# Optimization experiments

Hardware: AMD Instinct MI355X
Metric: run time of the kernel (lower is better)

## Reference

```python
import jax, jax.numpy as jnp
import numpy as np

N, H, E, T = 100000, 128, 500000, 6  # nodes, hidden, max edges, edge types


def setup_inputs() -> dict:
    key = jax.random.key(0)
    ks = jax.random.split(key, 16)
    xav_e = float(np.sqrt(6.0 / (H + T * H)))  # xavier_uniform for edge_dense
    xav_h = float(np.sqrt(6.0 / (H + H)))
    u = lambda k, s, a: jax.random.uniform(k, s, jnp.float32, -a, a)
    return {
        "node_embeddings": jax.random.normal(ks[0], (N, H), jnp.float32),
        "W_edge": u(ks[1], (H, T * H), xav_e),
        "b_edge": 1e-6 * jax.random.normal(ks[2], (T * H,), jnp.float32),
        "W_ir": u(ks[3], (H, H), xav_h), "b_ir": jnp.zeros((H,), jnp.float32),
        "W_iz": u(ks[4], (H, H), xav_h), "b_iz": jnp.zeros((H,), jnp.float32),
        "W_in": u(ks[5], (H, H), xav_h), "b_in": jnp.zeros((H,), jnp.float32),
        "W_hr": u(ks[6], (H, H), xav_h),
        "W_hz": u(ks[7], (H, H), xav_h),
        "W_hn": u(ks[8], (H, H), xav_h), "b_hn": jnp.zeros((H,), jnp.float32),
        "source_indices": jax.random.randint(ks[9], (E,), 0, N, jnp.int32),
        "dest_indices": jax.random.randint(ks[10], (E,), 0, N, jnp.int32),
        "edge_types": jax.random.randint(ks[11], (E,), 0, T, jnp.int32),
        "num_edges": 450000,
    }


def reference(node_embeddings, W_edge, b_edge, W_ir, b_ir, W_iz, b_iz,
              W_in, b_in, W_hr, W_hz, W_hn, b_hn,
              source_indices, dest_indices, edge_types, num_edges):
    num_nodes, hidden = node_embeddings.shape
    max_edges = edge_types.shape[0]
    # gather source nodes, project to all edge types at once: [E, T*H]
    src = node_embeddings[source_indices]
    all_types = (src @ W_edge + b_edge).reshape(max_edges, -1, hidden)  # [E,T,H]
    # select per-edge type
    msg = jnp.take_along_axis(all_types, edge_types[:, None, None], axis=1)[:, 0, :]
    # mask padding edges, scatter-add into destination nodes
    msg = jnp.where((jnp.arange(max_edges) < num_edges)[:, None], msg, 0)
    agg = jax.ops.segment_sum(msg, dest_indices, num_segments=num_nodes)
    # GRU update: carry h = aggregated messages, inputs x = node_embeddings
    h, x = agg, node_embeddings
    r = jax.nn.sigmoid(x @ W_ir + b_ir + h @ W_hr)
    z = jax.nn.sigmoid(x @ W_iz + b_iz + h @ W_hz)
    n = jnp.tanh(x @ W_in + b_in + r * (h @ W_hn + b_hn))
    return (1.0 - z) * n + z * h
```

## Files before the change

kernel.cpp:

```cpp
#include <hip/hip_runtime.h>
#include <hip/hip_bf16.h>

#define HD 128
#define NT 6

typedef unsigned short u16;
typedef unsigned int u32;
typedef __attribute__((ext_vector_type(8))) short bf16x8;
typedef __attribute__((ext_vector_type(4))) float f32x4;

__device__ __forceinline__ float sigmoidf_(float x) {
  return 1.0f / (1.0f + __expf(-x));
}

__device__ __forceinline__ u16 f2bf(float x) {
  u32 u = __float_as_uint(x);
  return (u16)((u + 0x7FFFu + ((u >> 16) & 1u)) >> 16);
}
__device__ __forceinline__ float bflo(u32 v) { return __uint_as_float(v << 16); }
__device__ __forceinline__ float bfhi(u32 v) { return __uint_as_float(v & 0xffff0000u); }

__device__ __forceinline__ int swz(int p) { return p ^ (((p >> 8) & 7) << 4); }

__global__ void k_cvt_w(const float* __restrict__ We,
                        const float* __restrict__ Wir, const float* __restrict__ Wiz,
                        const float* __restrict__ Win, const float* __restrict__ Whr,
                        const float* __restrict__ Whz, const float* __restrict__ Whn,
                        u16* __restrict__ WeT, u16* __restrict__ WgT) {
  int i = blockIdx.x * blockDim.x + threadIdx.x;
  if (i < NT * HD * HD) {
    int c = i >> 7, k = i & 127;
    WeT[i] = f2bf(We[(size_t)k * (NT * HD) + c]);
  } else {
    int j = i - NT * HD * HD;
    if (j < 6 * HD * HD) {
      int m = j >> 14, jj = j & 16383;
      int c = jj >> 7, k = jj & 127;
      const float* W = (m == 0) ? Wir : (m == 1) ? Wiz : (m == 2) ? Win
                     : (m == 3) ? Whr : (m == 4) ? Whz : Whn;
      WgT[j] = f2bf(W[(size_t)k * HD + c]);
    }
  }
}

__global__ __launch_bounds__(256) void k_gemm_edge6(
    const float* __restrict__ X, const u16* __restrict__ WeT,
    const float* __restrict__ Be, u16* __restrict__ P, int N)
{
  __shared__ char As[32768];
  __shared__ char Bs[32768];
  const int tid = threadIdx.x;
  const int row0 = blockIdx.x * 128;

  #pragma unroll
  for (int i = 0; i < 8; ++i) {
    int p = i * 4096 + tid * 16;
    int row = row0 + (p >> 8);
    union { u16 u[8]; bf16x8 v; } ra;
    if (row < N) {
      const float4* s = (const float4*)(X + (size_t)row0 * HD + (p >> 1));
      float4 f0 = s[0], f1 = s[1];
      ra.u[0] = f2bf(f0.x); ra.u[1] = f2bf(f0.y); ra.u[2] = f2bf(f0.z); ra.u[3] = f2bf(f0.w);
      ra.u[4] = f2bf(f1.x); ra.u[5] = f2bf(f1.y); ra.u[6] = f2bf(f1.z); ra.u[7] = f2bf(f1.w);
    } else {
      #pragma unroll
      for (int j = 0; j < 8; ++j) ra.u[j] = 0;
    }
    *(bf16x8*)(As + swz(p)) = ra.v;
  }

  const int l = tid & 63, w = tid >> 6;
  const int m0 = (w >> 1) * 64, n0 = (w & 1) * 64;
  const int lr = l & 15, lg = l >> 4;
  f32x4 zero = {0.f, 0.f, 0.f, 0.f};

  for (int t = 0; t < NT; ++t) {
    __syncthreads();
    const char* gB = (const char*)(WeT + (size_t)t * HD * HD);
    #pragma unroll
    for (int i = 0; i < 8; ++i) {
      int p = i * 4096 + tid * 16;
      *(bf16x8*)(Bs + swz(p)) = *(const bf16x8*)(gB + p);
    }
    __syncthreads();

    f32x4 acc[4][4];
    #pragma unroll
    for (int m = 0; m < 4; ++m)
      #pragma unroll
      for (int n = 0; n < 4; ++n) acc[m][n] = zero;

    #pragma unroll
    for (int k = 0; k < 4; ++k) {
      bf16x8 a[4], b[4];
      #pragma unroll
      for (int m = 0; m < 4; ++m)
        a[m] = *(const bf16x8*)(As + swz((m0 + m * 16 + lr) * 256 + k * 64 + lg * 16));
      #pragma unroll
      for (int n = 0; n < 4; ++n)
        b[n] = *(const bf16x8*)(Bs + swz((n0 + n * 16 + lr) * 256 + k * 64 + lg * 16));
      #pragma unroll
      for (int m = 0; m < 4; ++m)
        #pragma unroll
        for (int n = 0; n < 4; ++n)
          acc[m][n] = __builtin_amdgcn_mfma_f32_16x16x32_bf16(a[m], b[n], acc[m][n], 0, 0, 0);
    }

    float bias[4];
    #pragma unroll
    for (int n = 0; n < 4; ++n) bias[n] = Be[t * HD + n0 + n * 16 + lr];
    #pragma unroll
    for (int m = 0; m < 4; ++m) {
      int rbase = row0 + m0 + m * 16 + lg * 4;
      #pragma unroll
      for (int j = 0; j < 4; ++j) {
        int row = rbase + j;
        if (row < N) {
          #pragma unroll
          for (int n = 0; n < 4; ++n)
            P[(size_t)row * (NT * HD) + t * HD + n0 + n * 16 + lr] =
                f2bf(acc[m][n][j] + bias[n]);
        }
      }
    }
  }
}

__global__ __launch_bounds__(256) void k_count(const int* __restrict__ dst,
                                               const int* __restrict__ nePtr,
                                               int* __restrict__ deg) {
  const int ne = nePtr[0];
  for (int e = blockIdx.x * blockDim.x + threadIdx.x; e < ne;
       e += gridDim.x * blockDim.x)
    atomicAdd(&deg[dst[e]], 1);
}

__global__ __launch_bounds__(256) void k_scan_a(const int* __restrict__ deg,
                                                int* __restrict__ off,
                                                int* __restrict__ bsum, int N) {
  __shared__ int s[256];
  const int b = blockIdx.x, tid = threadIdx.x;
  const int base = b * 1024 + tid * 4;
  int v0 = 0, v1 = 0, v2 = 0, v3 = 0;
  if (base < N) v0 = deg[base];
  if (base + 1 < N) v1 = deg[base + 1];
  if (base + 2 < N) v2 = deg[base + 2];
  if (base + 3 < N) v3 = deg[base + 3];
  const int sum = v0 + v1 + v2 + v3;
  s[tid] = sum;
  __syncthreads();
  for (int d = 1; d < 256; d <<= 1) {
    int t = (tid >= d) ? s[tid - d] : 0;
    __syncthreads();
    s[tid] += t;
    __syncthreads();
  }
  const int excl = s[tid] - sum;
  if (base < N) off[base] = excl;
  if (base + 1 < N) off[base + 1] = excl + v0;
  if (base + 2 < N) off[base + 2] = excl + v0 + v1;
  if (base + 3 < N) off[base + 3] = excl + v0 + v1 + v2;
  if (tid == 255) bsum[b] = s[255];
}

__global__ void k_scan_b(int* __restrict__ bsum, int nb) {
  __shared__ int s[1024];
  const int tid = threadIdx.x;
  const int v = (tid < nb) ? bsum[tid] : 0;
  s[tid] = v;
  __syncthreads();
  for (int d = 1; d < 1024; d <<= 1) {
    int t = (tid >= d) ? s[tid - d] : 0;
    __syncthreads();
    s[tid] += t;
    __syncthreads();
  }
  if (tid < nb) bsum[tid] = s[tid] - v;
}

__global__ __launch_bounds__(256) void k_scan_c(int* __restrict__ off,
                                                const int* __restrict__ bsum, int N) {
  const int b = blockIdx.x, tid = threadIdx.x;
  const int add = bsum[b];
  const int base = b * 1024 + tid * 4;
  #pragma unroll
  for (int i = 0; i < 4; ++i)
    if (base + i < N) off[base + i] += add;
}

__global__ __launch_bounds__(256) void k_fill(const int* __restrict__ src,
                                              const int* __restrict__ dst,
                                              const int* __restrict__ typ,
                                              const int* __restrict__ nePtr,
                                              int* __restrict__ off,
                                              u32* __restrict__ elist) {
  const int ne = nePtr[0];
  for (int e = blockIdx.x * blockDim.x + threadIdx.x; e < ne;
       e += gridDim.x * blockDim.x) {
    int pos = atomicAdd(&off[dst[e]], 1);
    elist[pos] = (u32)(src[e] * NT + typ[e]);
  }
}

__global__ __launch_bounds__(256) void k_gather(
    const u16* __restrict__ P, const int* __restrict__ deg,
    const int* __restrict__ off, const u32* __restrict__ elist,
    u16* __restrict__ Hb, int N)
{
  const int l = threadIdx.x & 63;
  int wid = (int)((blockIdx.x * blockDim.x + threadIdx.x) >> 6);
  int nw = (int)((gridDim.x * blockDim.x) >> 6);
  for (int n = wid; n < N; n += nw) {
    const int e1 = off[n];
    const int e0 = e1 - deg[n];
    float a0 = 0.f, a1 = 0.f, b0 = 0.f, b1 = 0.f;
    for (int e = e0; e < e1; e += 4) {
      u32 p0 = elist[e];
      u32 p1 = (e + 1 < e1) ? elist[e + 1] : p0;
      u32 p2 = (e + 2 < e1) ? elist[e + 2] : p0;
      u32 p3 = (e + 3 < e1) ? elist[e + 3] : p0;
      u32 v0 = *((const u32*)(P + (size_t)p0 * HD) + l);
      u32 v1 = *((const u32*)(P + (size_t)p1 * HD) + l);
      u32 v2 = *((const u32*)(P + (size_t)p2 * HD) + l);
      u32 v3 = *((const u32*)(P + (size_t)p3 * HD) + l);
      if (e + 1 >= e1) v1 = 0;
      if (e + 2 >= e1) v2 = 0;
      if (e + 3 >= e1) v3 = 0;
      a0 += bflo(v0); a1 += bfhi(v0);
      b0 += bflo(v1); b1 += bfhi(v1);
      a0 += bflo(v2); a1 += bfhi(v2);
      b0 += bflo(v3); b1 += bfhi(v3);
    }
    a0 += b0; a1 += b1;
    u32 hp = ((u32)f2bf(a1) << 16) | (u32)f2bf(a0);
    *((u32*)(Hb + (size_t)n * HD) + l) = hp;
  }
}

__global__ __launch_bounds__(512, 2) void k_gru3(
    const float* __restrict__ X, const u16* __restrict__ Hb,
    const u16* __restrict__ WgT,
    const float* __restrict__ bir, const float* __restrict__ biz,
    const float* __restrict__ bin_, const float* __restrict__ bhn,
    float* __restrict__ out, int N)
{
  __shared__ char Xs[32768];
  __shared__ char Hs[32768];
  __shared__ char Wb[2][32768];
  const int tid = threadIdx.x;
  const int row0 = blockIdx.x * 128;
  const int l = tid & 63, w = tid >> 6;
  const int lr = l & 15, lg = l >> 4;
  const int rloc = w * 16;

  #pragma unroll
  for (int i = 0; i < 4; ++i) {
    int p = i * 8192 + tid * 16;
    int row = row0 + (p >> 8);
    union { u16 u[8]; bf16x8 v; } rx, rh;
    if (row < N) {
      const float4* sx = (const float4*)(X + (size_t)row0 * HD + (p >> 1));
      float4 x0 = sx[0], x1 = sx[1];
      rx.u[0] = f2bf(x0.x); rx.u[1] = f2bf(x0.y); rx.u[2] = f2bf(x0.z); rx.u[3] = f2bf(x0.w);
      rx.u[4] = f2bf(x1.x); rx.u[5] = f2bf(x1.y); rx.u[6] = f2bf(x1.z); rx.u[7] = f2bf(x1.w);
      rh.v = *(const bf16x8*)((const char*)Hb + (size_t)row0 * 256 + p);
    } else {
      #pragma unroll
      for (int j = 0; j < 8; ++j) { rx.u[j] = 0; rh.u[j] = 0; }
    }
    *(bf16x8*)(Xs + swz(p)) = rx.v;
    *(bf16x8*)(Hs + swz(p)) = rh.v;
  }

  bf16x8 wreg[4];
  auto loadW = [&](int g) {
    const char* gp = (const char*)(WgT + (size_t)g * HD * HD);
    #pragma unroll
    for (int i = 0; i < 4; ++i)
      wreg[i] = *(const bf16x8*)(gp + i * 8192 + tid * 16);
  };
  auto writeW = [&](int buf) {
    #pragma unroll
    for (int i = 0; i < 4; ++i) {
      int p = i * 8192 + tid * 16;
      *(bf16x8*)(Wb[buf] + swz(p)) = wreg[i];
    }
  };

  f32x4 zero = {0.f, 0.f, 0.f, 0.f};
  auto sweepL = [&](const char* Ab, const char* Wp, f32x4* acc) {
    #pragma unroll
    for (int n = 0; n < 8; ++n) acc[n] = zero;
    #pragma unroll
    for (int k = 0; k < 4; ++k) {
      bf16x8 a = *(const bf16x8*)(Ab + swz((rloc + lr) * 256 + k * 64 + lg * 16));
      #pragma unroll
      for (int n = 0; n < 8; ++n) {
        bf16x8 b = *(const bf16x8*)(Wp + swz((n * 16 + lr) * 256 + k * 64 + lg * 16));
        acc[n] = __builtin_amdgcn_mfma_f32_16x16x32_bf16(a, b, acc[n], 0, 0, 0);
      }
    }
  };

  f32x4 t1[8], t2[8], rg[8], nn[8];
  float bv[8];

  loadW(0); writeW(0);
  __syncthreads();

  loadW(3);
  sweepL(Xs, Wb[0], t1);
  writeW(1);
  __syncthreads();

  loadW(5);
  sweepL(Hs, Wb[1], t2);
  writeW(0);
  #pragma unroll
  for (int n = 0; n < 8; ++n) bv[n] = bir[n * 16 + lr];
  #pragma unroll
  for (int n = 0; n < 8; ++n)
    #pragma unroll
    for (int j = 0; j < 4; ++j) rg[n][j] = sigmoidf_(t1[n][j] + bv[n] + t2[n][j]);
  __syncthreads();

  loadW(2);
  sweepL(Hs, Wb[0], t2);
  writeW(1);
  #pragma unroll
  for (int n = 0; n < 8; ++n) bv[n] = bhn[n * 16 + lr];
  #pragma unroll
  for (int n = 0; n < 8; ++n)
    #pragma unroll
    for (int j = 0; j < 4; ++j) rg[n][j] *= (t2[n][j] + bv[n]);
  __syncthreads();

  loadW(1);
  sweepL(Xs, Wb[1], t1);
  writeW(0);
  #pragma unroll
  for (int n = 0; n < 8; ++n) bv[n] = bin_[n * 16 + lr];
  #pragma unroll
  for (int n = 0; n < 8; ++n)
    #pragma unroll
    for (int j = 0; j < 4; ++j) nn[n][j] = tanhf(t1[n][j] + bv[n] + rg[n][j]);
  __syncthreads();

  loadW(4);
  sweepL(Xs, Wb[0], t1);
  writeW(1);
  __syncthreads();

  sweepL(Hs, Wb[1], t2);
  #pragma unroll
  for (int n = 0; n < 8; ++n) bv[n] = biz[n * 16 + lr];
  #pragma unroll
  for (int n = 0; n < 8; ++n) {
    #pragma unroll
    for (int j = 0; j < 4; ++j) {
      int row = row0 + rloc + lg * 4 + j;
      if (row < N) {
        int col = n * 16 + lr;
        float z = sigmoidf_(t1[n][j] + bv[n] + t2[n][j]);
        u16 hu = Hb[(size_t)row * HD + col];
        float h = __uint_as_float((u32)hu << 16);
        out[(size_t)row * HD + col] = (1.0f - z) * nn[n][j] + z * h;
      }
    }
  }
}

__global__ __launch_bounds__(256) void k_gather_gru(
    const float* __restrict__ X, const u16* __restrict__ P,
    const int* __restrict__ deg, const int* __restrict__ off,
    const u32* __restrict__ elist, const u16* __restrict__ WgT,
    const float* __restrict__ bir, const float* __restrict__ biz,
    const float* __restrict__ bin_, const float* __restrict__ bhn,
    float* __restrict__ out, int N)
{
  __shared__ char Xs[16384];
  __shared__ char Hs[16384];
  const int tid = threadIdx.x;
  const int l = tid & 63, w = tid >> 6;
  const int row0 = blockIdx.x * 64;
  const int wr0 = w * 16;

  #pragma unroll
  for (int it = 0; it < 4; ++it) {
    int chunk = it * 64 + l;
    int r = chunk >> 4, seg = chunk & 15;
    int grow = row0 + wr0 + r;
    union { u16 u[8]; bf16x8 v; } rx;
    if (grow < N) {
      const float4* sx = (const float4*)(X + (size_t)grow * HD + seg * 8);
      float4 x0 = sx[0], x1 = sx[1];
      rx.u[0] = f2bf(x0.x); rx.u[1] = f2bf(x0.y); rx.u[2] = f2bf(x0.z); rx.u[3] = f2bf(x0.w);
      rx.u[4] = f2bf(x1.x); rx.u[5] = f2bf(x1.y); rx.u[6] = f2bf(x1.z); rx.u[7] = f2bf(x1.w);
    } else {
      #pragma unroll
      for (int j = 0; j < 8; ++j) rx.u[j] = 0;
    }
    *(bf16x8*)(Xs + swz((wr0 + r) * 256 + seg * 16)) = rx.v;
  }

  for (int i = 0; i < 16; ++i) {
    int n = row0 + wr0 + i;
    float a0 = 0.f, a1 = 0.f;
    if (n < N) {
      int e1 = off[n];
      for (int e = e1 - deg[n]; e < e1; e += 4) {
        u32 p0 = elist[e];
        u32 p1 = (e + 1 < e1) ? elist[e + 1] : p0;
        u32 p2 = (e + 2 < e1) ? elist[e + 2] : p0;
        u32 p3 = (e + 3 < e1) ? elist[e + 3] : p0;
        u32 v0 = *((const u32*)(P + (size_t)p0 * HD) + l);
        u32 v1 = *((const u32*)(P + (size_t)p1 * HD) + l);
        u32 v2 = *((const u32*)(P + (size_t)p2 * HD) + l);
        u32 v3 = *((const u32*)(P + (size_t)p3 * HD) + l);
        if (e + 1 >= e1) v1 = 0;
        if (e + 2 >= e1) v2 = 0;
        if (e + 3 >= e1) v3 = 0;
        a0 += bflo(v0) + bflo(v1) + bflo(v2) + bflo(v3);
        a1 += bfhi(v0) + bfhi(v1) + bfhi(v2) + bfhi(v3);
      }
    }
    u32 hp = ((u32)f2bf(a1) << 16) | (u32)f2bf(a0);
    *(u32*)(Hs + swz((wr0 + i) * 256 + l * 4)) = hp;
  }

  const int lr = l & 15, lg = l >> 4;
  const int rloc = wr0;

  f32x4 zero = {0.f, 0.f, 0.f, 0.f};
  auto sweep = [&](const char* Ab, const u16* WT, f32x4* acc) {
    #pragma unroll
    for (int n = 0; n < 8; ++n) acc[n] = zero;
    #pragma unroll
    for (int k = 0; k < 4; ++k) {
      bf16x8 a = *(const bf16x8*)(Ab + swz((rloc + lr) * 256 + k * 64 + lg * 16));
      #pragma unroll
      for (int n = 0; n < 8; ++n) {
        bf16x8 b = *(const bf16x8*)(WT + (size_t)(n * 16 + lr) * HD + k * 32 + lg * 8);
        acc[n] = __builtin_amdgcn_mfma_f32_16x16x32_bf16(a, b, acc[n], 0, 0, 0);
      }
    }
  };

  f32x4 t1[8], t2[8], rg[8], nn[8];
  float bv[8];

  sweep(Xs, WgT + 0 * HD * HD, t1);
  sweep(Hs, WgT + 3 * HD * HD, t2);
  #pragma unroll
  for (int n = 0; n < 8; ++n) bv[n] = bir[n * 16 + lr];
  #pragma unroll
  for (int n = 0; n < 8; ++n)
    #pragma unroll
    for (int j = 0; j < 4; ++j) rg[n][j] = sigmoidf_(t1[n][j] + bv[n] + t2[n][j]);

  sweep(Hs, WgT + 5 * HD * HD, t2);
  #pragma unroll
  for (int n = 0; n < 8; ++n) bv[n] = bhn[n * 16 + lr];
  #pragma unroll
  for (int n = 0; n < 8; ++n)
    #pragma unroll
    for (int j = 0; j < 4; ++j) rg[n][j] *= (t2[n][j] + bv[n]);

  sweep(Xs, WgT + 2 * HD * HD, t1);
  #pragma unroll
  for (int n = 0; n < 8; ++n) bv[n] = bin_[n * 16 + lr];
  #pragma unroll
  for (int n = 0; n < 8; ++n)
    #pragma unroll
    for (int j = 0; j < 4; ++j) nn[n][j] = tanhf(t1[n][j] + bv[n] + rg[n][j]);

  sweep(Xs, WgT + 1 * HD * HD, t1);
  sweep(Hs, WgT + 4 * HD * HD, t2);
  #pragma unroll
  for (int n = 0; n < 8; ++n) bv[n] = biz[n * 16 + lr];
  #pragma unroll
  for (int n = 0; n < 8; ++n) {
    #pragma unroll
    for (int j = 0; j < 4; ++j) {
      int row = row0 + rloc + lg * 4 + j;
      if (row < N) {
        float z = sigmoidf_(t1[n][j] + bv[n] + t2[n][j]);
        u16 hu = *(const u16*)(Hs + swz((rloc + lg * 4 + j) * 256 + (n * 16 + lr) * 2));
        float h = __uint_as_float((u32)hu << 16);
        out[(size_t)row * HD + n * 16 + lr] = (1.0f - z) * nn[n][j] + z * h;
      }
    }
  }
}

__global__ __launch_bounds__(256) void k_scatter(
    const u16* __restrict__ P, const int* __restrict__ src,
    const int* __restrict__ dst, const int* __restrict__ typ,
    const int* __restrict__ nePtr, float* __restrict__ agg,
    int ldP, int fixedType)
{
  const int ne = nePtr[0];
  const int lane = threadIdx.x & 63;
  const int wid = (int)((blockIdx.x * blockDim.x + threadIdx.x) >> 6);
  const int nw = (int)((gridDim.x * blockDim.x) >> 6);
  for (int e = wid; e < ne; e += nw) {
    const int t = typ[e];
    if (fixedType >= 0 && t != fixedType) continue;
    const size_t po = (ldP == HD) ? (size_t)src[e] * HD
                                  : (size_t)src[e] * (NT * HD) + (size_t)t * HD;
    u32 v = *(const u32*)(P + po + lane * 2);
    float* o = agg + (size_t)dst[e] * HD + lane * 2;
    unsafeAtomicAdd(o, bflo(v));
    unsafeAtomicAdd(o + 1, bfhi(v));
  }
}

__global__ __launch_bounds__(256) void k_gru(
    const float* __restrict__ X, const float* __restrict__ agg,
    const u16* __restrict__ WgT,
    const float* __restrict__ bir, const float* __restrict__ biz,
    const float* __restrict__ bin_, const float* __restrict__ bhn,
    float* __restrict__ out, int N)
{
  __shared__ char Xs[16384];
  __shared__ char Hs[16384];
  const int tid = threadIdx.x;
  const int row0 = blockIdx.x * 64;

  #pragma unroll
  for (int i = 0; i < 4; ++i) {
    int p = i * 4096 + tid * 16;
    int row = row0 + (p >> 8);
    union { u16 u[8]; bf16x8 v; } rx, rh;
    if (row < N) {
      const float4* sx = (const float4*)(X + (size_t)row0 * HD + (p >> 1));
      const float4* sh = (const float4*)(agg + (size_t)row0 * HD + (p >> 1));
      float4 x0 = sx[0], x1 = sx[1], h0 = sh[0], h1 = sh[1];
      rx.u[0] = f2bf(x0.x); rx.u[1] = f2bf(x0.y); rx.u[2] = f2bf(x0.z); rx.u[3] = f2bf(x0.w);
      rx.u[4] = f2bf(x1.x); rx.u[5] = f2bf(x1.y); rx.u[6] = f2bf(x1.z); rx.u[7] = f2bf(x1.w);
      rh.u[0] = f2bf(h0.x); rh.u[1] = f2bf(h0.y); rh.u[2] = f2bf(h0.z); rh.u[3] = f2bf(h0.w);
      rh.u[4] = f2bf(h1.x); rh.u[5] = f2bf(h1.y); rh.u[6] = f2bf(h1.z); rh.u[7] = f2bf(h1.w);
    } else {
      #pragma unroll
      for (int j = 0; j < 8; ++j) { rx.u[j] = 0; rh.u[j] = 0; }
    }
    *(bf16x8*)(Xs + swz(p)) = rx.v;
    *(bf16x8*)(Hs + swz(p)) = rh.v;
  }
  __syncthreads();

  const int l = tid & 63, w = tid >> 6;
  const int lr = l & 15, lg = l >> 4;
  const int rloc = w * 16;

  f32x4 zero = {0.f, 0.f, 0.f, 0.f};
  auto sweep = [&](const char* Ab, const u16* WT, f32x4* acc) {
    #pragma unroll
    for (int n = 0; n < 8; ++n) acc[n] = zero;
    #pragma unroll
    for (int k = 0; k < 4; ++k) {
      bf16x8 a = *(const bf16x8*)(Ab + swz((rloc + lr) * 256 + k * 64 + lg * 16));
      #pragma unroll
      for (int n = 0; n < 8; ++n) {
        bf16x8 b = *(const bf16x8*)(WT + (size_t)(n * 16 + lr) * HD + k * 32 + lg * 8);
        acc[n] = __builtin_amdgcn_mfma_f32_16x16x32_bf16(a, b, acc[n], 0, 0, 0);
      }
    }
  };

  f32x4 t1[8], t2[8], rg[8], nn[8];
  float bv[8];

  sweep(Xs, WgT + 0 * HD * HD, t1);
  sweep(Hs, WgT + 3 * HD * HD, t2);
  #pragma unroll
  for (int n = 0; n < 8; ++n) bv[n] = bir[n * 16 + lr];
  #pragma unroll
  for (int n = 0; n < 8; ++n)
    #pragma unroll
    for (int j = 0; j < 4; ++j) rg[n][j] = sigmoidf_(t1[n][j] + bv[n] + t2[n][j]);

  sweep(Hs, WgT + 5 * HD * HD, t2);
  #pragma unroll
  for (int n = 0; n < 8; ++n) bv[n] = bhn[n * 16 + lr];
  #pragma unroll
  for (int n = 0; n < 8; ++n)
    #pragma unroll
    for (int j = 0; j < 4; ++j) rg[n][j] *= (t2[n][j] + bv[n]);

  sweep(Xs, WgT + 2 * HD * HD, t1);
  #pragma unroll
  for (int n = 0; n < 8; ++n) bv[n] = bin_[n * 16 + lr];
  #pragma unroll
  for (int n = 0; n < 8; ++n)
    #pragma unroll
    for (int j = 0; j < 4; ++j) nn[n][j] = tanhf(t1[n][j] + bv[n] + rg[n][j]);

  sweep(Xs, WgT + 1 * HD * HD, t1);
  sweep(Hs, WgT + 4 * HD * HD, t2);
  #pragma unroll
  for (int n = 0; n < 8; ++n) bv[n] = biz[n * 16 + lr];
  #pragma unroll
  for (int n = 0; n < 8; ++n) {
    #pragma unroll
    for (int j = 0; j < 4; ++j) {
      int row = row0 + rloc + lg * 4 + j;
      if (row < N) {
        float z = sigmoidf_(t1[n][j] + bv[n] + t2[n][j]);
        float h = agg[(size_t)row * HD + n * 16 + lr];
        out[(size_t)row * HD + n * 16 + lr] = (1.0f - z) * nn[n][j] + z * h;
      }
    }
  }
}

extern "C" void kernel_launch(void* const* d_in, const int* in_sizes, int n_in,
                              void* d_out, int out_size, void* d_ws, size_t ws_size,
                              hipStream_t stream) {
  const float* X      = (const float*)d_in[0];
  const float* W_edge = (const float*)d_in[1];
  const float* b_edge = (const float*)d_in[2];
  const float* b_ir   = (const float*)d_in[4];
  const float* b_iz   = (const float*)d_in[6];
  const float* b_in   = (const float*)d_in[8];
  const float* b_hn   = (const float*)d_in[12];
  const int* src      = (const int*)d_in[13];
  const int* dst      = (const int*)d_in[14];
  const int* typ      = (const int*)d_in[15];
  const int* nePtr    = (const int*)d_in[16];

  const int N = in_sizes[0] / HD;
  const int E = in_sizes[13];
  char* ws = (char*)d_ws;

  size_t cur = 0;
  auto alloc = [&](size_t bytes) {
    size_t p = cur;
    cur = (cur + bytes + 255) & ~(size_t)255;
    return p;
  };
  u16* WeT   = (u16*)(ws + alloc((size_t)NT * HD * HD * 2));
  u16* WgT   = (u16*)(ws + alloc((size_t)6 * HD * HD * 2));
  int* deg   = (int*)(ws + alloc((size_t)N * 4));
  int* offA  = (int*)(ws + alloc((size_t)N * 4));
  int* bsum  = (int*)(ws + alloc(1024 * 4));
  u32* elist = (u32*)(ws + alloc((size_t)E * 4));
  size_t base_need = cur;
  u16* P     = (u16*)(ws + alloc((size_t)N * NT * HD * 2));
  const size_t csr_need = cur;
  u16* Hb    = (u16*)(ws + alloc((size_t)N * HD * 2));
  const size_t split_need = cur;

  const int gb = (N + 127) / 128;
  const int NB = (N + 1023) / 1024;

  k_cvt_w<<<(NT * HD * HD + 6 * HD * HD + 255) / 256, 256, 0, stream>>>(
      W_edge, (const float*)d_in[3], (const float*)d_in[5], (const float*)d_in[7],
      (const float*)d_in[9], (const float*)d_in[10], (const float*)d_in[11], WeT, WgT);

  if (ws_size >= csr_need) {
    hipMemsetAsync(deg, 0, (size_t)N * 4, stream);
    k_gemm_edge6<<<gb, 256, 0, stream>>>(X, WeT, b_edge, P, N);
    k_count<<<1024, 256, 0, stream>>>(dst, nePtr, deg);
    k_scan_a<<<NB, 256, 0, stream>>>(deg, offA, bsum, N);
    k_scan_b<<<1, 1024, 0, stream>>>(bsum, NB);
    k_scan_c<<<NB, 256, 0, stream>>>(offA, bsum, N);
    k_fill<<<1024, 256, 0, stream>>>(src, dst, typ, nePtr, offA, elist);
    if (ws_size >= split_need) {
      k_gather<<<(N + 3) / 4, 256, 0, stream>>>(P, deg, offA, elist, Hb, N);
      k_gru3<<<gb, 512, 0, stream>>>(
          X, Hb, WgT, b_ir, b_iz, b_in, b_hn, (float*)d_out, N);
    } else {
      k_gather_gru<<<(N + 63) / 64, 256, 0, stream>>>(
          X, P, deg, offA, elist, WgT, b_ir, b_iz, b_in, b_hn, (float*)d_out, N);
    }
  } else {
    float* agg = (float*)d_out;
    hipMemsetAsync(d_out, 0, (size_t)out_size * sizeof(float), stream);
    size_t pneed = base_need + (size_t)N * NT * HD * 2;
    if (ws_size >= pneed) {
      u16* Pf = (u16*)(ws + base_need);
      k_gemm_edge6<<<gb, 256, 0, stream>>>(X, WeT, b_edge, Pf, N);
      k_scatter<<<2048, 256, 0, stream>>>(Pf, src, dst, typ, nePtr, agg, NT * HD, -1);
      k_gru<<<(N + 63) / 64, 256, 0, stream>>>(X, agg, WgT, b_ir, b_iz, b_in, b_hn, agg, N);
    }
  }
}
```

Measured before the change: 253.6 us.

## Emit bf16 copy of node embeddings in edge GEMM and use LDS-free GRU kernel

The edge-projection GEMM now also writes a bf16 copy of the node embeddings into workspace while it converts them. A new GRU kernel, k_gru4, reads that bf16 copy and the aggregated bf16 H directly from global memory into MFMA operands, with no shared-memory staging, in 32x64 wave tiles. The goal is to halve the X read traffic in the GRU stage and drop the LDS staging and barriers of k_gru3. In exchange it adds an extra write of X in bf16 and relies on cache hits for the repeated weight and activation loads across gate passes.

```diff
diff --git a/kernel.cpp b/kernel.cpp
--- a/kernel.cpp
+++ b/kernel.cpp
@@ -45,7 +45,8 @@
 
 __global__ __launch_bounds__(256) void k_gemm_edge6(
     const float* __restrict__ X, const u16* __restrict__ WeT,
-    const float* __restrict__ Be, u16* __restrict__ P, int N)
+    const float* __restrict__ Be, u16* __restrict__ P,
+    u16* __restrict__ Xb, int N)
 {
   __shared__ char As[32768];
   __shared__ char Bs[32768];
@@ -62,6 +63,7 @@
       float4 f0 = s[0], f1 = s[1];
       ra.u[0] = f2bf(f0.x); ra.u[1] = f2bf(f0.y); ra.u[2] = f2bf(f0.z); ra.u[3] = f2bf(f0.w);
       ra.u[4] = f2bf(f1.x); ra.u[5] = f2bf(f1.y); ra.u[6] = f2bf(f1.z); ra.u[7] = f2bf(f1.w);
+      if (Xb) *(bf16x8*)((char*)Xb + (size_t)row * 256 + (p & 255)) = ra.v;
     } else {
       #pragma unroll
       for (int j = 0; j < 8; ++j) ra.u[j] = 0;
@@ -237,6 +239,118 @@
   }
 }
 
+__global__ __launch_bounds__(256) void k_gru4(
+    const u16* __restrict__ Xb, const u16* __restrict__ Hb,
+    const u16* __restrict__ WgT,
+    const float* __restrict__ bir, const float* __restrict__ biz,
+    const float* __restrict__ bin_, const float* __restrict__ bhn,
+    float* __restrict__ out, int N)
+{
+  const int tid = threadIdx.x;
+  const int l = tid & 63;
+  const int lr = l & 15, lg = l >> 4;
+  const int gw = (int)(blockIdx.x * 4 + (tid >> 6));
+  const int R0 = (gw >> 1) * 32;
+  const int C0 = (gw & 1) * 64;
+  if (R0 >= N) return;
+
+  const bf16x8 zf = {0, 0, 0, 0, 0, 0, 0, 0};
+  f32x4 zero = {0.f, 0.f, 0.f, 0.f};
+
+  auto ldA = [&](const u16* Mb, int m, int kc) -> bf16x8 {
+    int row = R0 + m * 16 + lr;
+    if (row >= N) return zf;
+    return *(const bf16x8*)(Mb + (size_t)row * HD + kc * 32 + lg * 8);
+  };
+  auto ldB = [&](const u16* Wt, int n, int kc) -> bf16x8 {
+    return *(const bf16x8*)(Wt + (size_t)(C0 + n * 16 + lr) * HD + kc * 32 + lg * 8);
+  };
+
+  f32x4 t[2][4];
+  auto zeroT = [&]() {
+    #pragma unroll
+    for (int m = 0; m < 2; ++m)
+      #pragma unroll
+      for (int n = 0; n < 4; ++n) t[m][n] = zero;
+  };
+  auto pass = [&](const u16* Mb, const u16* Wt) {
+    #pragma unroll
+    for (int kc = 0; kc < 4; ++kc) {
+      bf16x8 a0 = ldA(Mb, 0, kc);
+      bf16x8 a1 = ldA(Mb, 1, kc);
+      #pragma unroll
+      for (int n = 0; n < 4; ++n) {
+        bf16x8 b = ldB(Wt, n, kc);
+        t[0][n] = __builtin_amdgcn_mfma_f32_16x16x32_bf16(a0, b, t[0][n], 0, 0, 0);
+        t[1][n] = __builtin_amdgcn_mfma_f32_16x16x32_bf16(a1, b, t[1][n], 0, 0, 0);
+      }
+    }
+  };
+
+  float bv[4];
+  auto ldBias = [&](const float* bp) {
+    #pragma unroll
+    for (int n = 0; n < 4; ++n) bv[n] = bp[C0 + n * 16 + lr];
+  };
+
+  float rg[2][4][4], nn[2][4][4];
+
+  zeroT();
+  pass(Xb, WgT + 0 * HD * HD);
+  pass(Hb, WgT + 3 * HD * HD);
+  ldBias(bir);
+  #pragma unroll
+  for (int m = 0; m < 2; ++m)
+    #pragma unroll
+    for (int n = 0; n < 4; ++n)
+      #pragma unroll
+      for (int j = 0; j < 4; ++j)
+        rg[m][n][j] = sigmoidf_(t[m][n][j] + bv[n]);
+
+  zeroT();
+  pass(Hb, WgT + 5 * HD * HD);
+  ldBias(bhn);
+  #pragma unroll
+  for (int m = 0; m < 2; ++m)
+    #pragma unroll
+    for (int n = 0; n < 4; ++n)
+      #pragma unroll
+      for (int j = 0; j < 4; ++j)
+        rg[m][n][j] *= (t[m][n][j] + bv[n]);
+
+  zeroT();
+  pass(Xb, WgT + 2 * HD * HD);
+  ldBias(bin_);
+  #pragma unroll
+  for (int m = 0; m < 2; ++m)
+    #pragma unroll
+    for (int n = 0; n < 4; ++n)
+      #pragma unroll
+      for (int j = 0; j < 4; ++j)
+        nn[m][n][j] = tanhf(t[m][n][j] + bv[n] + rg[m][n][j]);
+
+  zeroT();
+  pass(Xb, WgT + 1 * HD * HD);
+  pass(Hb, WgT + 4 * HD * HD);
+  ldBias(biz);
+  #pragma unroll
+  for (int m = 0; m < 2; ++m) {
+    #pragma unroll
+    for (int j = 0; j < 4; ++j) {
+      int row = R0 + m * 16 + lg * 4 + j;
+      if (row < N) {
+        #pragma unroll
+        for (int n = 0; n < 4; ++n) {
+          int col = C0 + n * 16 + lr;
+          float z = sigmoidf_(t[m][n][j] + bv[n]);
+          float h = __uint_as_float((u32)Hb[(size_t)row * HD + col] << 16);
+          out[(size_t)row * HD + col] = (1.0f - z) * nn[m][n][j] + z * h;
+        }
+      }
+    }
+  }
+}
+
 __global__ __launch_bounds__(512, 2) void k_gru3(
     const float* __restrict__ X, const u16* __restrict__ Hb,
     const u16* __restrict__ WgT,
@@ -650,6 +764,8 @@
   const size_t csr_need = cur;
   u16* Hb    = (u16*)(ws + alloc((size_t)N * HD * 2));
   const size_t split_need = cur;
+  u16* Xb    = (u16*)(ws + alloc((size_t)N * HD * 2));
+  const size_t xb_need = cur;
 
   const int gb = (N + 127) / 128;
   const int NB = (N + 1023) / 1024;
@@ -659,14 +775,20 @@
       (const float*)d_in[9], (const float*)d_in[10], (const float*)d_in[11], WeT, WgT);
 
   if (ws_size >= csr_need) {
+    const bool haveXb = (ws_size >= xb_need);
     hipMemsetAsync(deg, 0, (size_t)N * 4, stream);
-    k_gemm_edge6<<<gb, 256, 0, stream>>>(X, WeT, b_edge, P, N);
+    k_gemm_edge6<<<gb, 256, 0, stream>>>(X, WeT, b_edge, P, haveXb ? Xb : (u16*)nullptr, N);
     k_count<<<1024, 256, 0, stream>>>(dst, nePtr, deg);
     k_scan_a<<<NB, 256, 0, stream>>>(deg, offA, bsum, N);
     k_scan_b<<<1, 1024, 0, stream>>>(bsum, NB);
     k_scan_c<<<NB, 256, 0, stream>>>(offA, bsum, N);
     k_fill<<<1024, 256, 0, stream>>>(src, dst, typ, nePtr, offA, elist);
-    if (ws_size >= split_need) {
+    if (haveXb) {
+      k_gather<<<(N + 3) / 4, 256, 0, stream>>>(P, deg, offA, elist, Hb, N);
+      const int nWaves = ((N + 31) / 32) * 2;
+      k_gru4<<<(nWaves + 3) / 4, 256, 0, stream>>>(
+          Xb, Hb, WgT, b_ir, b_iz, b_in, b_hn, (float*)d_out, N);
+    } else if (ws_size >= split_need) {
       k_gather<<<(N + 3) / 4, 256, 0, stream>>>(P, deg, offA, elist, Hb, N);
       k_gru3<<<gb, 512, 0, stream>>>(
           X, Hb, WgT, b_ir, b_iz, b_in, b_hn, (float*)d_out, N);
@@ -680,7 +802,7 @@
     size_t pneed = base_need + (size_t)N * NT * HD * 2;
     if (ws_size >= pneed) {
       u16* Pf = (u16*)(ws + base_need);
-      k_gemm_edge6<<<gb, 256, 0, stream>>>(X, WeT, b_edge, Pf, N);
+      k_gemm_edge6<<<gb, 256, 0, stream>>>(X, WeT, b_edge, Pf, (u16*)nullptr, N);
       k_scatter<<<2048, 256, 0, stream>>>(Pf, src, dst, typ, nePtr, agg, NT * HD, -1);
       k_gru<<<(N + 63) / 64, 256, 0, stream>>>(X, agg, WgT, b_ir, b_iz, b_in, b_hn, agg, N);
     }
```

Result: slower. 308.5 us (+21.7%).

## Fold GRU input projections into edge GEMM and add lighter GRU kernel

Applied to the files above, without the earlier changes.

The edge-projection GEMM now runs 9 weight tiles per row block instead of 6. It also computes the x@W_ir/W_iz/W_in projections (with biases) and writes them to a bf16 Gx buffer, reusing the X tile already staged in LDS. A new k_gru5 kernel then does only the three hidden-side matmuls, reading Gx and Hb from global memory. This removes the X reload and half the GRU MFMA work from the final kernel. In exchange it writes and reads 3*N*H bf16 values and needs extra workspace, with a fallback path kept when that workspace is missing.

```diff
diff --git a/kernel.cpp b/kernel.cpp
--- a/kernel.cpp
+++ b/kernel.cpp
@@ -19,6 +19,7 @@
 }
 __device__ __forceinline__ float bflo(u32 v) { return __uint_as_float(v << 16); }
 __device__ __forceinline__ float bfhi(u32 v) { return __uint_as_float(v & 0xffff0000u); }
+__device__ __forceinline__ float bfs(u16 v) { return __uint_as_float((u32)v << 16); }
 
 __device__ __forceinline__ int swz(int p) { return p ^ (((p >> 8) & 7) << 4); }
 
@@ -26,13 +27,20 @@
                         const float* __restrict__ Wir, const float* __restrict__ Wiz,
                         const float* __restrict__ Win, const float* __restrict__ Whr,
                         const float* __restrict__ Whz, const float* __restrict__ Whn,
-                        u16* __restrict__ WeT, u16* __restrict__ WgT) {
+                        u16* __restrict__ WeT9, u16* __restrict__ WgT) {
   int i = blockIdx.x * blockDim.x + threadIdx.x;
-  if (i < NT * HD * HD) {
-    int c = i >> 7, k = i & 127;
-    WeT[i] = f2bf(We[(size_t)k * (NT * HD) + c]);
+  if (i < 9 * HD * HD) {
+    int m = i >> 14, jj = i & 16383;
+    int c = jj >> 7, k = jj & 127;
+    float v;
+    if (m < 6) v = We[(size_t)k * (NT * HD) + m * HD + c];
+    else {
+      const float* W = (m == 6) ? Wir : (m == 7) ? Wiz : Win;
+      v = W[(size_t)k * HD + c];
+    }
+    WeT9[i] = f2bf(v);
   } else {
-    int j = i - NT * HD * HD;
+    int j = i - 9 * HD * HD;
     if (j < 6 * HD * HD) {
       int m = j >> 14, jj = j & 16383;
       int c = jj >> 7, k = jj & 127;
@@ -45,7 +53,10 @@
 
 __global__ __launch_bounds__(256) void k_gemm_edge6(
     const float* __restrict__ X, const u16* __restrict__ WeT,
-    const float* __restrict__ Be, u16* __restrict__ P, int N)
+    const float* __restrict__ Be,
+    const float* __restrict__ bir, const float* __restrict__ biz,
+    const float* __restrict__ bin_,
+    u16* __restrict__ P, u16* __restrict__ Gx, int N, int nt)
 {
   __shared__ char As[32768];
   __shared__ char Bs[32768];
@@ -74,7 +85,7 @@
   const int lr = l & 15, lg = l >> 4;
   f32x4 zero = {0.f, 0.f, 0.f, 0.f};
 
-  for (int t = 0; t < NT; ++t) {
+  for (int t = 0; t < nt; ++t) {
     __syncthreads();
     const char* gB = (const char*)(WeT + (size_t)t * HD * HD);
     #pragma unroll
@@ -106,9 +117,12 @@
           acc[m][n] = __builtin_amdgcn_mfma_f32_16x16x32_bf16(a[m], b[n], acc[m][n], 0, 0, 0);
     }
 
+    const float* bp = (t < 6) ? (Be + t * HD)
+                    : (t == 6) ? bir : (t == 7) ? biz : bin_;
     float bias[4];
     #pragma unroll
-    for (int n = 0; n < 4; ++n) bias[n] = Be[t * HD + n0 + n * 16 + lr];
+    for (int n = 0; n < 4; ++n) bias[n] = bp[n0 + n * 16 + lr];
+
     #pragma unroll
     for (int m = 0; m < 4; ++m) {
       int rbase = row0 + m0 + m * 16 + lg * 4;
@@ -116,10 +130,17 @@
       for (int j = 0; j < 4; ++j) {
         int row = rbase + j;
         if (row < N) {
-          #pragma unroll
-          for (int n = 0; n < 4; ++n)
-            P[(size_t)row * (NT * HD) + t * HD + n0 + n * 16 + lr] =
-                f2bf(acc[m][n][j] + bias[n]);
+          if (t < 6) {
+            #pragma unroll
+            for (int n = 0; n < 4; ++n)
+              P[(size_t)row * (NT * HD) + t * HD + n0 + n * 16 + lr] =
+                  f2bf(acc[m][n][j] + bias[n]);
+          } else {
+            u16* op = Gx + (size_t)(t - 6) * N * HD;
+            #pragma unroll
+            for (int n = 0; n < 4; ++n)
+              op[(size_t)row * HD + n0 + n * 16 + lr] = f2bf(acc[m][n][j] + bias[n]);
+          }
         }
       }
     }
@@ -237,6 +258,110 @@
   }
 }
 
+__global__ __launch_bounds__(256) void k_gru5(
+    const u16* __restrict__ Hb, const u16* __restrict__ WgT,
+    const u16* __restrict__ Gx,
+    const float* __restrict__ bhn,
+    float* __restrict__ out, int N)
+{
+  __shared__ char Wb[2][32768];
+  const int tid = threadIdx.x;
+  const int l = tid & 63, w = tid >> 6;
+  const int lr = l & 15, lg = l >> 4;
+  const int rw = blockIdx.x * 64 + w * 16;
+  const size_t NH = (size_t)N * HD;
+  const u16* Gxr = Gx;
+  const u16* Gxz = Gx + NH;
+  const u16* Gxn = Gx + 2 * NH;
+
+  bf16x8 wreg[8];
+  auto loadW = [&](int g) {
+    const char* gp = (const char*)(WgT + (size_t)g * HD * HD);
+    #pragma unroll
+    for (int i = 0; i < 8; ++i)
+      wreg[i] = *(const bf16x8*)(gp + i * 4096 + tid * 16);
+  };
+  auto writeW = [&](int buf) {
+    #pragma unroll
+    for (int i = 0; i < 8; ++i) {
+      int p = i * 4096 + tid * 16;
+      *(bf16x8*)(Wb[buf] + swz(p)) = wreg[i];
+    }
+  };
+
+  const bf16x8 zf = {0, 0, 0, 0, 0, 0, 0, 0};
+  f32x4 zero = {0.f, 0.f, 0.f, 0.f};
+  f32x4 t2[8];
+  auto sweep = [&](const char* Wp) {
+    #pragma unroll
+    for (int n = 0; n < 8; ++n) t2[n] = zero;
+    const int arow = rw + lr;
+    #pragma unroll
+    for (int kc = 0; kc < 4; ++kc) {
+      bf16x8 a = (arow < N) ? *(const bf16x8*)(Hb + (size_t)arow * HD + kc * 32 + lg * 8)
+                            : zf;
+      #pragma unroll
+      for (int n = 0; n < 8; ++n) {
+        bf16x8 b = *(const bf16x8*)(Wp + swz((n * 16 + lr) * 256 + kc * 64 + lg * 16));
+        t2[n] = __builtin_amdgcn_mfma_f32_16x16x32_bf16(a, b, t2[n], 0, 0, 0);
+      }
+    }
+  };
+
+  float s[8][4];
+  float bvn[8];
+  #pragma unroll
+  for (int n = 0; n < 8; ++n) bvn[n] = bhn[n * 16 + lr];
+
+  loadW(3); writeW(0);
+  loadW(5);
+  __syncthreads();
+
+  sweep(Wb[0]);
+  writeW(1);
+  loadW(4);
+  #pragma unroll
+  for (int n = 0; n < 8; ++n) {
+    #pragma unroll
+    for (int j = 0; j < 4; ++j) {
+      int row = rw + lg * 4 + j;
+      float g = (row < N) ? bfs(Gxr[(size_t)row * HD + n * 16 + lr]) : 0.f;
+      s[n][j] = sigmoidf_(g + t2[n][j]);
+    }
+  }
+  __syncthreads();
+
+  sweep(Wb[1]);
+  writeW(0);
+  #pragma unroll
+  for (int n = 0; n < 8; ++n) {
+    #pragma unroll
+    for (int j = 0; j < 4; ++j) {
+      int row = rw + lg * 4 + j;
+      float g = (row < N) ? bfs(Gxn[(size_t)row * HD + n * 16 + lr]) : 0.f;
+      float rn = s[n][j] * (t2[n][j] + bvn[n]);
+      s[n][j] = tanhf(g + rn);
+    }
+  }
+  __syncthreads();
+
+  sweep(Wb[0]);
+  #pragma unroll
+  for (int n = 0; n < 8; ++n) {
+    #pragma unroll
+    for (int j = 0; j < 4; ++j) {
+      int row = rw + lg * 4 + j;
+      if (row < N) {
+        int col = n * 16 + lr;
+        float g = bfs(Gxz[(size_t)row * HD + col]);
+        float z = sigmoidf_(g + t2[n][j]);
+        float h = bfs(Hb[(size_t)row * HD + col]);
+        out[(size_t)row * HD + col] = (1.0f - z) * s[n][j] + z * h;
+      }
+    }
+  }
+}
+
 __global__ __launch_bounds__(512, 2) void k_gru3(
     const float* __restrict__ X, const u16* __restrict__ Hb,
     const u16* __restrict__ WgT,
@@ -362,8 +487,7 @@
       if (row < N) {
         int col = n * 16 + lr;
         float z = sigmoidf_(t1[n][j] + bv[n] + t2[n][j]);
-        u16 hu = Hb[(size_t)row * HD + col];
-        float h = __uint_as_float((u32)hu << 16);
+        float h = bfs(Hb[(size_t)row * HD + col]);
         out[(size_t)row * HD + col] = (1.0f - z) * nn[n][j] + z * h;
       }
     }
@@ -486,8 +610,7 @@
       if (row < N) {
         float z = sigmoidf_(t1[n][j] + bv[n] + t2[n][j]);
         u16 hu = *(const u16*)(Hs + swz((rloc + lg * 4 + j) * 256 + (n * 16 + lr) * 2));
-        float h = __uint_as_float((u32)hu << 16);
-        out[(size_t)row * HD + n * 16 + lr] = (1.0f - z) * nn[n][j] + z * h;
+        out[(size_t)row * HD + n * 16 + lr] = (1.0f - z) * nn[n][j] + z * bfs(hu);
       }
     }
   }
@@ -639,7 +762,7 @@
     cur = (cur + bytes + 255) & ~(size_t)255;
     return p;
   };
-  u16* WeT   = (u16*)(ws + alloc((size_t)NT * HD * HD * 2));
+  u16* WeT9  = (u16*)(ws + alloc((size_t)9 * HD * HD * 2));
   u16* WgT   = (u16*)(ws + alloc((size_t)6 * HD * HD * 2));
   int* deg   = (int*)(ws + alloc((size_t)N * 4));
   int* offA  = (int*)(ws + alloc((size_t)N * 4));
@@ -650,23 +773,33 @@
   const size_t csr_need = cur;
   u16* Hb    = (u16*)(ws + alloc((size_t)N * HD * 2));
   const size_t split_need = cur;
+  u16* Gx    = (u16*)(ws + alloc((size_t)3 * N * HD * 2));
+  const size_t gx_need = cur;
 
   const int gb = (N + 127) / 128;
   const int NB = (N + 1023) / 1024;
 
-  k_cvt_w<<<(NT * HD * HD + 6 * HD * HD + 255) / 256, 256, 0, stream>>>(
+  k_cvt_w<<<((9 + 6) * HD * HD + 255) / 256, 256, 0, stream>>>(
       W_edge, (const float*)d_in[3], (const float*)d_in[5], (const float*)d_in[7],
-      (const float*)d_in[9], (const float*)d_in[10], (const float*)d_in[11], WeT, WgT);
+      (const float*)d_in[9], (const float*)d_in[10], (const float*)d_in[11], WeT9, WgT);
 
   if (ws_size >= csr_need) {
+    const bool haveGx = (ws_size >= gx_need);
+    const bool haveHb = (ws_size >= split_need);
     hipMemsetAsync(deg, 0, (size_t)N * 4, stream);
-    k_gemm_edge6<<<gb, 256, 0, stream>>>(X, WeT, b_edge, P, N);
+    k_gemm_edge6<<<gb, 256, 0, stream>>>(X, WeT9, b_edge, b_ir, b_iz, b_in,
+                                         P, haveGx ? Gx : (u16*)nullptr, N,
+                                         haveGx ? 9 : 6);
     k_count<<<1024, 256, 0, stream>>>(dst, nePtr, deg);
     k_scan_a<<<NB, 256, 0, stream>>>(deg, offA, bsum, N);
     k_scan_b<<<1, 1024, 0, stream>>>(bsum, NB);
     k_scan_c<<<NB, 256, 0, stream>>>(offA, bsum, N);
     k_fill<<<1024, 256, 0, stream>>>(src, dst, typ, nePtr, offA, elist);
-    if (ws_size >= split_need) {
+    if (haveGx) {
+      k_gather<<<(N + 3) / 4, 256, 0, stream>>>(P, deg, offA, elist, Hb, N);
+      k_gru5<<<(N + 63) / 64, 256, 0, stream>>>(
+          Hb, WgT, Gx, b_hn, (float*)d_out, N);
+    } else if (haveHb) {
       k_gather<<<(N + 3) / 4, 256, 0, stream>>>(P, deg, offA, elist, Hb, N);
       k_gru3<<<gb, 512, 0, stream>>>(
           X, Hb, WgT, b_ir, b_iz, b_in, b_hn, (float*)d_out, N);
@@ -680,7 +813,8 @@
     size_t pneed = base_need + (size_t)N * NT * HD * 2;
     if (ws_size >= pneed) {
       u16* Pf = (u16*)(ws + base_need);
-      k_gemm_edge6<<<gb, 256, 0, stream>>>(X, WeT, b_edge, Pf, N);
+      k_gemm_edge6<<<gb, 256, 0, stream>>>(X, WeT9, b_edge, b_ir, b_iz, b_in,
+                                           Pf, (u16*)nullptr, N, 6);
       k_scatter<<<2048, 256, 0, stream>>>(Pf, src, dst, typ, nePtr, agg, NT * HD, -1);
       k_gru<<<(N + 63) / 64, 256, 0, stream>>>(X, agg, WgT, b_ir, b_iz, b_in, b_hn, agg, N);
     }
```

Measured after the change: 410.4 us. +61.8%, slower.

## Keep GRU A-operands in registers and shrink blocks to 64 rows

Applied to the files above, without the earlier changes.

The GRU kernel no longer stages X and H tiles in shared memory. Each lane now loads its MFMA A-fragments for X and H straight from global memory into registers, and blocks shrink from 512 threads/128 rows to 256 threads/64 rows. This removes 64KB of LDS per block and the A-operand LDS reads, which should allow more resident blocks. The cost is that each weight matrix is staged into LDS twice as often per row, plus higher register pressure from the held fragments.

```diff
diff --git a/kernel.cpp b/kernel.cpp
--- a/kernel.cpp
+++ b/kernel.cpp
@@ -19,6 +19,7 @@
 }
 __device__ __forceinline__ float bflo(u32 v) { return __uint_as_float(v << 16); }
 __device__ __forceinline__ float bfhi(u32 v) { return __uint_as_float(v & 0xffff0000u); }
+__device__ __forceinline__ float bfs(u16 v) { return __uint_as_float((u32)v << 16); }
 
 __device__ __forceinline__ int swz(int p) { return p ^ (((p >> 8) & 7) << 4); }
 
@@ -237,67 +238,63 @@
   }
 }
 
-__global__ __launch_bounds__(512, 2) void k_gru3(
+__global__ __launch_bounds__(256) void k_gru6(
     const float* __restrict__ X, const u16* __restrict__ Hb,
     const u16* __restrict__ WgT,
     const float* __restrict__ bir, const float* __restrict__ biz,
     const float* __restrict__ bin_, const float* __restrict__ bhn,
     float* __restrict__ out, int N)
 {
-  __shared__ char Xs[32768];
-  __shared__ char Hs[32768];
   __shared__ char Wb[2][32768];
   const int tid = threadIdx.x;
-  const int row0 = blockIdx.x * 128;
   const int l = tid & 63, w = tid >> 6;
   const int lr = l & 15, lg = l >> 4;
-  const int rloc = w * 16;
-
-  #pragma unroll
-  for (int i = 0; i < 4; ++i) {
-    int p = i * 8192 + tid * 16;
-    int row = row0 + (p >> 8);
-    union { u16 u[8]; bf16x8 v; } rx, rh;
-    if (row < N) {
-      const float4* sx = (const float4*)(X + (size_t)row0 * HD + (p >> 1));
+  const int rw = blockIdx.x * 64 + w * 16;
+  const int arow = rw + lr;
+
+  const bf16x8 zf = {0, 0, 0, 0, 0, 0, 0, 0};
+  bf16x8 Xa[4], Ha[4];
+  if (arow < N) {
+    #pragma unroll
+    for (int kc = 0; kc < 4; ++kc) {
+      const float4* sx = (const float4*)(X + (size_t)arow * HD + kc * 32 + lg * 8);
       float4 x0 = sx[0], x1 = sx[1];
+      union { u16 u[8]; bf16x8 v; } rx;
       rx.u[0] = f2bf(x0.x); rx.u[1] = f2bf(x0.y); rx.u[2] = f2bf(x0.z); rx.u[3] = f2bf(x0.w);
       rx.u[4] = f2bf(x1.x); rx.u[5] = f2bf(x1.y); rx.u[6] = f2bf(x1.z); rx.u[7] = f2bf(x1.w);
-      rh.v = *(const bf16x8*)((const char*)Hb + (size_t)row0 * 256 + p);
-    } else {
-      #pragma unroll
-      for (int j = 0; j < 8; ++j) { rx.u[j] = 0; rh.u[j] = 0; }
-    }
-    *(bf16x8*)(Xs + swz(p)) = rx.v;
-    *(bf16x8*)(Hs + swz(p)) = rh.v;
-  }
-
-  bf16x8 wreg[4];
+      Xa[kc] = rx.v;
+      Ha[kc] = *(const bf16x8*)(Hb + (size_t)arow * HD + kc * 32 + lg * 8);
+    }
+  } else {
+    #pragma unroll
+    for (int kc = 0; kc < 4; ++kc) { Xa[kc] = zf; Ha[kc] = zf; }
+  }
+
+  bf16x8 wreg[8];
   auto loadW = [&](int g) {
     const char* gp = (const char*)(WgT + (size_t)g * HD * HD);
     #pragma unroll
-    for (int i = 0; i < 4; ++i)
-      wreg[i] = *(const bf16x8*)(gp + i * 8192 + tid * 16);
+    for (int i = 0; i < 8; ++i)
+      wreg[i] = *(const bf16x8*)(gp + i * 4096 + tid * 16);
   };
   auto writeW = [&](int buf) {
     #pragma unroll
-    for (int i = 0; i < 4; ++i) {
-      int p = i * 8192 + tid * 16;
+    for (int i = 0; i < 8; ++i) {
+      int p = i * 4096 + tid * 16;
       *(bf16x8*)(Wb[buf] + swz(p)) = wreg[i];
     }
   };
 
   f32x4 zero = {0.f, 0.f, 0.f, 0.f};
-  auto sweepL = [&](const char* Ab, const char* Wp, f32x4* acc) {
+  auto sweep = [&](const bf16x8* A, int buf, f32x4* acc) {
     #pragma unroll
     for (int n = 0; n < 8; ++n) acc[n] = zero;
     #pragma unroll
-    for (int k = 0; k < 4; ++k) {
-      bf16x8 a = *(const bf16x8*)(Ab + swz((rloc + lr) * 256 + k * 64 + lg * 16));
+    for (int kc = 0; kc < 4; ++kc) {
       #pragma unroll
       for (int n = 0; n < 8; ++n) {
-        bf16x8 b = *(const bf16x8*)(Wp + swz((n * 16 + lr) * 256 + k * 64 + lg * 16));
-        acc[n] = __builtin_amdgcn_mfma_f32_16x16x32_bf16(a, b, acc[n], 0, 0, 0);
+        bf16x8 b = *(const bf16x8*)(Wb[buf] + swz((n * 16 + lr) * 256 + kc * 64 + lg * 16));
+        acc[n] = __builtin_amdgcn_mfma_f32_16x16x32_bf16(A[kc], b, acc[n], 0, 0, 0);
       }
     }
   };
@@ -309,12 +306,12 @@
   __syncthreads();
 
   loadW(3);
-  sweepL(Xs, Wb[0], t1);
+  sweep(Xa, 0, t1);
   writeW(1);
   __syncthreads();
 
   loadW(5);
-  sweepL(Hs, Wb[1], t2);
+  sweep(Ha, 1, t2);
   writeW(0);
   #pragma unroll
   for (int n = 0; n < 8; ++n) bv[n] = bir[n * 16 + lr];
@@ -325,7 +322,7 @@
   __syncthreads();
 
   loadW(2);
-  sweepL(Hs, Wb[0], t2);
+  sweep(Ha, 0, t2);
   writeW(1);
   #pragma unroll
   for (int n = 0; n < 8; ++n) bv[n] = bhn[n * 16 + lr];
@@ -336,7 +333,7 @@
   __syncthreads();
 
   loadW(1);
-  sweepL(Xs, Wb[1], t1);
+  sweep(Xa, 1, t1);
   writeW(0);
   #pragma unroll
   for (int n = 0; n < 8; ++n) bv[n] = bin_[n * 16 + lr];
@@ -347,23 +344,22 @@
   __syncthreads();
 
   loadW(4);
-  sweepL(Xs, Wb[0], t1);
+  sweep(Xa, 0, t1);
   writeW(1);
   __syncthreads();
 
-  sweepL(Hs, Wb[1], t2);
+  sweep(Ha, 1, t2);
   #pragma unroll
   for (int n = 0; n < 8; ++n) bv[n] = biz[n * 16 + lr];
   #pragma unroll
   for (int n = 0; n < 8; ++n) {
     #pragma unroll
     for (int j = 0; j < 4; ++j) {
-      int row = row0 + rloc + lg * 4 + j;
+      int row = rw + lg * 4 + j;
       if (row < N) {
         int col = n * 16 + lr;
         float z = sigmoidf_(t1[n][j] + bv[n] + t2[n][j]);
-        u16 hu = Hb[(size_t)row * HD + col];
-        float h = __uint_as_float((u32)hu << 16);
+        float h = bfs(Hb[(size_t)row * HD + col]);
         out[(size_t)row * HD + col] = (1.0f - z) * nn[n][j] + z * h;
       }
     }
@@ -486,8 +482,7 @@
       if (row < N) {
         float z = sigmoidf_(t1[n][j] + bv[n] + t2[n][j]);
         u16 hu = *(const u16*)(Hs + swz((rloc + lg * 4 + j) * 256 + (n * 16 + lr) * 2));
-        float h = __uint_as_float((u32)hu << 16);
-        out[(size_t)row * HD + n * 16 + lr] = (1.0f - z) * nn[n][j] + z * h;
+        out[(size_t)row * HD + n * 16 + lr] = (1.0f - z) * nn[n][j] + z * bfs(hu);
       }
     }
   }
@@ -668,7 +663,7 @@
     k_fill<<<1024, 256, 0, stream>>>(src, dst, typ, nePtr, offA, elist);
     if (ws_size >= split_need) {
       k_gather<<<(N + 3) / 4, 256, 0, stream>>>(P, deg, offA, elist, Hb, N);
-      k_gru3<<<gb, 512, 0, stream>>>(
+      k_gru6<<<(N + 63) / 64, 256, 0, stream>>>(
           X, Hb, WgT, b_ir, b_iz, b_in, b_hn, (float*)d_out, N);
     } else {
       k_gather_gru<<<(N + 63) / 64, 256, 0, stream>>>(
```

Result: slower. 273.2 us (+7.7%).
